# Performance work log

Measured on AMD Instinct MI355X. Metric: run time of the kernel, lower is better.

The kernel has to match this reference:

```python
import jax, jax.numpy as jnp
import numpy as np

KSIZE = 3
KN = (KSIZE - 1) // 2  # 1
TEMP = 50.0


def _extract_patches(x, same_pad):
    """TF tf.image.extract_patches ordering: per location, (dy, dx, channel).
    x: [b,H,W,d] -> [b,h,w,9*d] (h=H,w=W if same_pad else H-2,W-2)."""
    if same_pad:
        x = jnp.pad(x, ((0, 0), (KN, KN), (KN, KN), (0, 0)))
    b, Hp, Wp, d = x.shape
    h, w = Hp - 2 * KN, Wp - 2 * KN
    slices = [x[:, dy:dy + h, dx:dx + w, :]
              for dy in range(KSIZE) for dx in range(KSIZE)]
    return jnp.concatenate(slices, axis=-1)


def setup_inputs() -> dict:
    key = jax.random.key(0)
    k1, k2, k3 = jax.random.split(key, 3)
    b, h, w, dims = 4, 48, 48, 64
    g_in = jax.random.normal(k1, (b, h, w, dims), dtype=jnp.float32)
    # binary inpainting mask (1 = known background, 0 = hole)
    mask = (jax.random.uniform(k2, (b, h, w, 1)) > 0.5).astype(jnp.float32)
    W2 = jax.random.normal(k3, (2 * dims, dims), dtype=jnp.float32) / np.sqrt(2.0 * dims)
    b2 = jnp.zeros((dims,), dtype=jnp.float32)
    return {"g_in": g_in, "mask": mask, "W2": W2, "b2": b2}


def reference(g_in, mask, W2, b2):
    b, h, w, dims = g_in.shape
    c = (h - 2 * KN) * (w - 2 * KN)

    mask_r = mask  # already (h,w,1); broadcasts over dims (== tile)
    bg = g_in * mask_r

    # p1: VALID 3x3 patches of bg -> dynamic kernels, [b, c, 9*dims]
    p1 = _extract_patches(bg, same_pad=False).reshape(b, c, KSIZE * KSIZE * dims)
    # p2: SAME 3x3 patches of g_in, [b, h, w, 9*dims]
    p2 = _extract_patches(g_in, same_pad=True)

    # cross-correlation: conv2d(ft, k1) == per-location dot with each bg patch
    CS = jnp.einsum('byxk,bjk->byxj', p2, p1)              # [b,h,w,c]
    k1d = jnp.sum(p1 * p1, axis=2)                          # [b,c]
    wwd = jnp.sum(p2 * p2, axis=3, keepdims=True)           # [b,h,w,1]
    DS1 = k1d[:, None, None, :] + wwd - 2.0 * CS            # squared distances
    mu = jnp.mean(DS1, axis=3, keepdims=True)
    sd = jnp.std(DS1, axis=3, keepdims=True)                # population std (tf.math.reduce_std)
    DS2 = -jnp.tanh((DS1 - mu) / sd)
    CA = jax.nn.softmax(TEMP * DS2, axis=-1)                # [b,h,w,c]

    # transposed conv aggregation with per-sample kernels k2[b,j,dy,dx,ch]
    k2 = p1.reshape(b, c, KSIZE, KSIZE, dims)
    CA_pad = jnp.pad(CA, ((0, 0), (KN, KN), (KN, KN), (0, 0)))
    acl = jnp.zeros((b, h, w, dims), dtype=g_in.dtype)
    for dy in range(KSIZE):
        for dx in range(KSIZE):
            win = CA_pad[:, 2 * KN - dy:2 * KN - dy + h, 2 * KN - dx:2 * KN - dx + w, :]
            acl = acl + jnp.einsum('byxj,bjd->byxd', win, k2[:, :, dy, dx, :])
    acl = acl / 9.0

    ACL = bg + acl * (1.0 - mask_r)
    con1 = jnp.concatenate([g_in, ACL], axis=3)             # [b,h,w,2*dims]
    return jax.nn.elu(jnp.einsum('byxk,kd->byxd', con1, W2) + b2)
```

## Files before the change

### kernel.cpp

```cpp
#include <hip/hip_runtime.h>
#include <hip/hip_fp16.h>
#include <math.h>

#define BB 4
#define HH 48
#define WW 48
#define DD 64
#define CC 2116
#define HWp (HH*WW)
#define PW 50
#define PP (PW*PW)

#define SLOTW 48
#define NSLOT 2208
#define NGRP 276
#define QW 2304
#define QROWS 2500

typedef __attribute__((ext_vector_type(8))) short short8;
typedef __attribute__((ext_vector_type(8))) _Float16 half8;
typedef __attribute__((ext_vector_type(4))) float float4v;

#define OFFB_GPAD  ((size_t)0)
#define OFFB_BGPAD ((size_t)1280000)
#define OFFB_E     ((size_t)2560000)
#define OFFB_K1D   ((size_t)2596864)
#define OFFB_BGT3  ((size_t)2632192)
#define OFFB_F     ((size_t)6023680)
#define OFFB_CA    ((size_t)52103680)
#define OFFB_CAY   ((size_t)92801536)
#define OFFB_ACLP  ((size_t)133499392)

__device__ __forceinline__ ushort f2bf(float x) {
    unsigned u = __float_as_uint(x);
    return (ushort)((u + 0x7FFFu + ((u >> 16) & 1u)) >> 16);
}

__device__ __forceinline__ float waveReduceSum(float x) {
#pragma unroll
    for (int o = 32; o > 0; o >>= 1) x += __shfl_down(x, o, 64);
    return x;
}

__device__ __forceinline__ __half2 u2h2(uint u) {
    union { uint u; __half2 h; } c; c.u = u; return c.h;
}
__device__ __forceinline__ uint h2u(__half2 h) {
    union { __half2 h; uint u; } c; c.h = h; return c.u;
}

__device__ __forceinline__ uint cvtpk_bf16(float lo, float hi) {
    uint r;
    asm("v_cvt_pk_bf16_f32 %0, %1, %2" : "=v"(r) : "v"(lo), "v"(hi));
    return r;
}

__device__ __forceinline__ float softexp(float d, float mu, float isd) {
    float z = (d - mu) * isd;
    float E2 = __expf(z + z);
    float r = __builtin_amdgcn_rcpf(E2 + 1.f);
    return __expf(fmaf(100.f, r, -50.f));
}

typedef __attribute__((address_space(3))) void lds_void_t;
typedef __attribute__((address_space(1))) void gmem_void_t;
__device__ __forceinline__ void gld16(const ushort* g, ushort* lds) {
    __builtin_amdgcn_global_load_lds((gmem_void_t*)g, (lds_void_t*)lds, 16, 0, 0);
}

__global__ __launch_bounds__(256) void build_pads(const float* __restrict__ g,
                                                  const float* __restrict__ mask,
                                                  ushort* __restrict__ gpad,
                                                  ushort* __restrict__ bgpad,
                                                  float* __restrict__ e) {
    int w = threadIdx.x >> 6, c = threadIdx.x & 63;
    int q4 = blockIdx.x * 4 + w;
    int b = q4 / PP, q = q4 % PP;
    int yp = q / PW, xp = q % PW;
    size_t o = (size_t)q4 * DD + c;
    if (yp >= 1 && yp <= HH && xp >= 1 && xp <= WW) {
        int pix = (yp - 1) * WW + (xp - 1);
        float gv = g[((size_t)b * HWp + pix) * DD + c];
        float m  = mask[(size_t)b * HWp + pix];
        float bgv = gv * m;
        gpad[o]  = f2bf(gv);
        bgpad[o] = f2bf(bgv);
        float ss = waveReduceSum(bgv * bgv);
        if (c == 0) e[b * HWp + pix] = ss;
    } else {
        gpad[o] = 0;
        bgpad[o] = 0;
    }
}

__global__ __launch_bounds__(256) void build_bgt3_k1d(const ushort* __restrict__ bgpad,
                                                      const float* __restrict__ e,
                                                      ushort* __restrict__ bgT3,
                                                      float* __restrict__ k1d) {
    int b = blockIdx.y;
    int t = threadIdx.x;
    if (blockIdx.x == 35) {
#pragma unroll 1
        for (int st = t; st < NSLOT; st += 256) {
            int jy = st / SLOTW, jx = st - jy * SLOTW;
            float s = 0.f;
            if (jx < 46) {
                const float* eb = e + (size_t)b * HWp + jy * WW + jx;
#pragma unroll
                for (int ddy = 0; ddy < 3; ddy++)
#pragma unroll
                    for (int ddx = 0; ddx < 3; ddx++) s += eb[ddy * WW + ddx];
            }
            k1d[(size_t)b * NSLOT + st] = s;
        }
        return;
    }
    __shared__ ushort T[66 * 65];
    int jt = blockIdx.x;
    const ushort* src = bgpad + (size_t)b * PP * DD;
    int lr = t >> 3, c8 = (t & 7) * 8;
#pragma unroll
    for (int pass = 0; pass < 2; pass++) {
        int r = lr + pass * 32;
        int v = jt * 64 + r;
        int vy = v / 48, vx = v - vy * 48;
        uint4 d = *(const uint4*)(src + (size_t)((vy + 1) * PW + (vx + 1)) * DD + c8);
        ushort tmp[8];
        *(uint4*)tmp = d;
#pragma unroll
        for (int u = 0; u < 8; u++) {
            float f = __uint_as_float((uint)tmp[u] << 16);
            __half h = __float2half_rn(f);
            T[r * 65 + c8 + u] = *(ushort*)&h;
        }
    }
    if (t < 16) {
        int r = 64 + (t >> 3);
        int c8b = (t & 7) * 8;
        int v = jt * 64 + r;
        int vy = v / 48, vx = v - vy * 48;
        uint4 d = *(const uint4*)(src + (size_t)((vy + 1) * PW + (vx + 1)) * DD + c8b);
        ushort tmp[8];
        *(uint4*)tmp = d;
#pragma unroll
        for (int u = 0; u < 8; u++) {
            float f = __uint_as_float((uint)tmp[u] << 16);
            __half h = __float2half_rn(f);
            T[r * 65 + c8b + u] = *(ushort*)&h;
        }
    }
    __syncthreads();
#pragma unroll
    for (int pass = 0; pass < 2; pass++) {
        int c = lr + pass * 32;
        int j8 = (t & 7) * 8;
        int col0 = jt * 64 + j8;
        if (col0 < NSLOT) {
#pragma unroll
            for (int dx = 0; dx < 3; dx++) {
                ushort tmp[8];
#pragma unroll
                for (int u = 0; u < 8; u++) tmp[u] = T[(j8 + u + dx) * 65 + c];
                *(uint4*)(bgT3 + ((size_t)b * 192 + dx * 64 + c) * NSLOT + col0) =
                    *(const uint4*)tmp;
            }
        }
    }
}

__global__ __launch_bounds__(256) void fgemm(const ushort* __restrict__ gpad,
                                             const ushort* __restrict__ bgpad,
                                             __half* __restrict__ Fout) {
    __shared__ ushort As[2 * 4096];
    __shared__ ushort Bs[2 * 4096];
    int i0 = blockIdx.x;
    int b = (i0 & 7) >> 1;
    int tile = ((i0 >> 3) << 1) | (i0 & 1);
    int ty = tile / 18, tx = tile - ty * 18;
    int m0 = ty * 128, n0 = tx * 128;
    const ushort* Ag = gpad + (size_t)b * PP * DD;
    const ushort* Bg = bgpad + (size_t)b * PP * DD;

    int tid = threadIdx.x;
    int l = tid & 63, w = tid >> 6;
    int quad = l >> 4, l15 = l & 15;
    int sw8 = (l15 >> 1) & 3;
    int wm = (w >> 1) * 64, wn = (w & 1) * 64;
    int rowInC = l >> 2;
    int cSw = (l & 3) ^ ((l >> 3) & 3);

    int baseA[2], baseB[2];
#pragma unroll
    for (int i = 0; i < 2; i++) {
        int rg = w * 2 + i;
        int r = rg * 16 + rowInC;
        int u = m0 + r; if (u > QROWS - 1) u = QROWS - 1;
        int n = n0 + r;
        int vy = n / 48, vx = n - vy * 48;
        baseA[i] = u * DD + cSw * 8;
        baseB[i] = ((vy + 1) * PW + (vx + 1)) * DD + cSw * 8;
    }

    float4v acc[4][4];
#pragma unroll
    for (int i = 0; i < 4; i++)
#pragma unroll
        for (int j = 0; j < 4; j++) acc[i][j] = (float4v){0.f, 0.f, 0.f, 0.f};

#pragma unroll
    for (int i = 0; i < 2; i++) {
        int rg = w * 2 + i;
        gld16(Ag + baseA[i], As + rg * 512);
        gld16(Bg + baseB[i], Bs + rg * 512);
    }

    int buf = 0;
    for (int k0 = 0; k0 < 192; k0 += 32) {
        __syncthreads();
        int nb = buf ^ 1;
        if (k0 + 32 < 192) {
#pragma unroll
            for (int i = 0; i < 2; i++) {
                int rg = w * 2 + i;
                gld16(Ag + baseA[i] + (k0 + 32), As + nb * 4096 + rg * 512);
                gld16(Bg + baseB[i] + (k0 + 32), Bs + nb * 4096 + rg * 512);
            }
        }
        const ushort* Ax = As + buf * 4096;
        const ushort* Bx = Bs + buf * 4096;
        short8 af[4], bf[4];
#pragma unroll
        for (int i = 0; i < 4; i++)
            af[i] = *(const short8*)&Ax[(wm + i * 16 + l15) * 32 + ((quad ^ sw8)) * 8];
#pragma unroll
        for (int j = 0; j < 4; j++)
            bf[j] = *(const short8*)&Bx[(wn + j * 16 + l15) * 32 + ((quad ^ sw8)) * 8];
#pragma unroll
        for (int i = 0; i < 4; i++)
#pragma unroll
            for (int j = 0; j < 4; j++)
                acc[i][j] = __builtin_amdgcn_mfma_f32_16x16x32_bf16(af[i], bf[j], acc[i][j], 0, 0, 0);
        buf = nb;
    }

    __half* C = Fout + (size_t)b * QROWS * QW;
#pragma unroll
    for (int i = 0; i < 4; i++) {
#pragma unroll
        for (int j = 0; j < 4; j++) {
            int n = n0 + wn + j * 16 + l15;
#pragma unroll
            for (int r = 0; r < 4; r++) {
                int m = m0 + wm + i * 16 + quad * 4 + r;
                if (m < QROWS) C[(size_t)m * QW + n] = __float2half(acc[i][j][r]);
            }
        }
    }
}

__global__ __launch_bounds__(320) void qrowsoft5(const __half* __restrict__ F,
                                                 const float* __restrict__ k1d,
                                                 ushort* __restrict__ CA) {
    __shared__ float red[8][321];
    int i0 = blockIdx.x;
    int b = (i0 & 7) >> 1;
    int sub = ((i0 >> 3) << 1) | (i0 & 1);
    int yq = sub / 48, x = sub - yq * 48;
    int y0 = yq * 4;

    int t = threadIdx.x;
    bool act = (t < NGRP);
    int jy = t / 6, jxb = (t - jy * 6) * 8;
    int slot0 = jy * SLOTW + jxb;
    bool vc6 = act && (jxb == 40);

    __half2 acc[4][4];
#pragma unroll
    for (int p = 0; p < 4; p++)
#pragma unroll
        for (int k = 0; k < 4; k++) acc[p][k] = u2h2(0u);

    float k1v[8] = {0.f, 0.f, 0.f, 0.f, 0.f, 0.f, 0.f, 0.f};

    if (act) {
        const float* k1 = k1d + (size_t)b * NSLOT + slot0;
        float4 ka = *(const float4*)k1;
        float4 kb = *(const float4*)(k1 + 4);
        k1v[0] = ka.x; k1v[1] = ka.y; k1v[2] = ka.z; k1v[3] = ka.w;
        k1v[4] = kb.x; k1v[5] = kb.y; k1v[6] = kb.z; k1v[7] = kb.w;

        const __half* Fb = F + ((size_t)b * QROWS + (size_t)y0 * PW + x) * QW + slot0;
#pragma unroll
        for (int r = 0; r < 6; r++) {
            const __half* R = Fb + (size_t)r * PW * QW;
#pragma unroll
            for (int dy = 0; dy < 3; dy++) {
                int p = r - dy;
                if (p >= 0 && p < 4) {
                    uint4 v4 = *(const uint4*)(R + 48 * dy);
                    acc[p][0] = __hadd2(acc[p][0], u2h2(v4.x));
                    acc[p][1] = __hadd2(acc[p][1], u2h2(v4.y));
                    acc[p][2] = __hadd2(acc[p][2], u2h2(v4.z));
                    acc[p][3] = __hadd2(acc[p][3], u2h2(v4.w));
                }
            }
        }
    }

    if (vc6) {
#pragma unroll
        for (int p = 0; p < 4; p++) acc[p][3] = u2h2(0u);
    }

#pragma unroll
    for (int p = 0; p < 4; p++) {
        float s1p = 0.f, s2p = 0.f;
#pragma unroll
        for (int k = 0; k < 4; k++) {
            float2 f = __half22float2(acc[p][k]);
            float d0 = k1v[2*k]   - 2.f * f.x;
            float d1 = k1v[2*k+1] - 2.f * f.y;
            s1p += d0 + d1;
            s2p = fmaf(d0, d0, fmaf(d1, d1, s2p));
        }
        red[p][t] = s1p;
        red[4 + p][t] = s2p;
    }
    __syncthreads();
    if (t < 128) {
        int v = t >> 4, sb = t & 15;
        float s = 0.f;
#pragma unroll
        for (int k = 0; k < 20; k++) s += red[v][sb + 16 * k];
#pragma unroll
        for (int o = 8; o > 0; o >>= 1) s += __shfl_down(s, o, 16);
        if (sb == 0) red[v][320] = s;
    }
    __syncthreads();
    float mu[4], isd[4];
#pragma unroll
    for (int p = 0; p < 4; p++) {
        float m = red[p][320] * (1.f / (float)CC);
        float ex2 = red[4 + p][320] * (1.f / (float)CC);
        mu[p] = m;
        isd[p] = rsqrtf(ex2 - m * m);
    }

    uint eb[4][4];
#pragma unroll
    for (int p = 0; p < 4; p++) {
        float es = 0.f;
#pragma unroll
        for (int k = 0; k < 4; k++) {
            float2 f = __half22float2(acc[p][k]);
            float d0 = k1v[2*k]   - 2.f * f.x;
            float d1 = k1v[2*k+1] - 2.f * f.y;
            if (k == 3 && vc6) { d0 = 1e9f; d1 = 1e9f; }
            float e0 = softexp(d0, mu[p], isd[p]);
            float e1 = softexp(d1, mu[p], isd[p]);
            es += e0 + e1;
            eb[p][k] = cvtpk_bf16(e0, e1);
        }
        red[p][t] = act ? es : 0.f;
    }
    __syncthreads();
    if (t < 64) {
        int v = t >> 4, sb = t & 15;
        float s = 0.f;
#pragma unroll
        for (int k = 0; k < 20; k++) s += red[v][sb + 16 * k];
#pragma unroll
        for (int o = 8; o > 0; o >>= 1) s += __shfl_down(s, o, 16);
        if (sb == 0) red[v][320] = s;
    }
    __syncthreads();

    if (act) {
#pragma unroll
        for (int p = 0; p < 4; p++) {
            float iz = __builtin_amdgcn_rcpf(red[p][320]);
            uint o[4];
#pragma unroll
            for (int k = 0; k < 4; k++) {
                uint wv = eb[p][k];
                float lo = __uint_as_float(wv << 16) * iz;
                float hi = __uint_as_float(wv & 0xffff0000u) * iz;
                __half2 hh = __halves2half2(__float2half_rn(lo), __float2half_rn(hi));
                o[k] = *(uint*)&hh;
            }
            int pix = (y0 + p) * WW + x;
            ushort* wp = CA + ((size_t)b * HWp + pix) * (size_t)NSLOT + slot0;
            *(uint4*)wp = *(const uint4*)o;
        }
    }
}

__global__ __launch_bounds__(320) void cay_k(const ushort* __restrict__ CAu,
                                             ushort* __restrict__ CAy) {
    int i0 = blockIdx.x;
    int b = (i0 & 7) >> 1;
    int sub = ((i0 >> 3) << 1) | (i0 & 1);
    int y = sub / 12, xt = sub - y * 12;
    int x0 = xt * 4;

    int t = threadIdx.x;
    if (t >= NGRP) return;
    int jy = t / 6, jxb = (t - jy * 6) * 8;
    int slot0 = jy * SLOTW + jxb;

    __half2 acc[4][4];
#pragma unroll
    for (int p = 0; p < 4; p++)
#pragma unroll
        for (int k = 0; k < 4; k++) acc[p][k] = u2h2(0u);

#pragma unroll
    for (int dy = 0; dy < 3; dy++) {
        int yy = y + 1 - dy;
        if (yy < 0 || yy >= 48) continue;
        if (jy < dy) continue;
        const ushort* rp = CAu + ((size_t)b * HWp + yy * 48 + x0) * (size_t)NSLOT
                         + slot0 - 48 * dy;
#pragma unroll
        for (int p = 0; p < 4; p++) {
            uint4 v4 = *(const uint4*)(rp + (size_t)p * NSLOT);
            acc[p][0] = __hadd2(acc[p][0], u2h2(v4.x));
            acc[p][1] = __hadd2(acc[p][1], u2h2(v4.y));
            acc[p][2] = __hadd2(acc[p][2], u2h2(v4.z));
            acc[p][3] = __hadd2(acc[p][3], u2h2(v4.w));
        }
    }

#pragma unroll
    for (int p = 0; p < 4; p++) {
        uint o[4];
#pragma unroll
        for (int k = 0; k < 4; k++) {
            __half2 h = acc[p][k];
            o[k] = *(uint*)&h;
        }
        *(uint4*)(CAy + ((size_t)b * HWp + y * 48 + x0 + p) * (size_t)NSLOT + slot0) =
            *(const uint4*)o;
    }
}

__global__ __launch_bounds__(256) void gemm4s(const ushort* __restrict__ Am,
                                              const ushort* __restrict__ Bm,
                                              __half* __restrict__ aclp) {
    __shared__ ushort As[2 * 4096];
    __shared__ ushort Bs[2 * 6144];
    int i0 = blockIdx.x;
    int b = (i0 & 7) >> 1;
    int t2 = ((i0 >> 3) << 1) | (i0 & 1);
    int s = t2 & 7, mt = t2 >> 3;
    int m0 = mt * 128;
    const int KB[9] = {0, 288, 576, 864, 1152, 1440, 1696, 1952, 2208};
    int kb = KB[s], ke = KB[s + 1];
    const ushort* Ab = Am + ((size_t)b * HWp + m0) * (size_t)NSLOT;
    const ushort* Bb = Bm + (size_t)b * 192 * (size_t)NSLOT;

    int tid = threadIdx.x;
    int l = tid & 63, w = tid >> 6;
    int quad = l >> 4, l15 = l & 15;
    int sw8 = (l15 >> 1) & 3;
    int wm = (w >> 1) * 64, wn = (w & 1) * 96;
    int rowInC = l >> 2;
    int cSw = (l & 3) ^ ((l >> 3) & 3);
    int cS8 = cSw * 8;

    float4v acc[4][6];
#pragma unroll
    for (int i = 0; i < 4; i++)
#pragma unroll
        for (int j = 0; j < 6; j++) acc[i][j] = (float4v){0.f, 0.f, 0.f, 0.f};

#pragma unroll
    for (int i = 0; i < 2; i++) {
        int rg = w * 2 + i;
        gld16(Ab + (size_t)(rg * 16 + rowInC) * NSLOT + kb + cS8, As + rg * 512);
    }
#pragma unroll
    for (int i = 0; i < 3; i++) {
        int rg = w * 3 + i;
        gld16(Bb + (size_t)(rg * 16 + rowInC) * NSLOT + kb + cS8, Bs + rg * 512);
    }

    int buf = 0;
    for (int k0 = kb; k0 < ke; k0 += 32) {
        __syncthreads();
        int nb = buf ^ 1;
        if (k0 + 32 < ke) {
#pragma unroll
            for (int i = 0; i < 2; i++) {
                int rg = w * 2 + i;
                gld16(Ab + (size_t)(rg * 16 + rowInC) * NSLOT + (k0 + 32) + cS8,
                      As + nb * 4096 + rg * 512);
            }
#pragma unroll
            for (int i = 0; i < 3; i++) {
                int rg = w * 3 + i;
                gld16(Bb + (size_t)(rg * 16 + rowInC) * NSLOT + (k0 + 32) + cS8,
                      Bs + nb * 6144 + rg * 512);
            }
        }
        const ushort* Ax = As + buf * 4096;
        const ushort* Bx = Bs + buf * 6144;
        half8 af[4], bf[6];
#pragma unroll
        for (int i = 0; i < 4; i++)
            af[i] = *(const half8*)&Ax[(wm + i * 16 + l15) * 32 + ((quad ^ sw8)) * 8];
#pragma unroll
        for (int j = 0; j < 6; j++)
            bf[j] = *(const half8*)&Bx[(wn + j * 16 + l15) * 32 + ((quad ^ sw8)) * 8];
#pragma unroll
        for (int i = 0; i < 4; i++)
#pragma unroll
            for (int j = 0; j < 6; j++)
                acc[i][j] = __builtin_amdgcn_mfma_f32_16x16x32_f16(af[i], bf[j], acc[i][j], 0, 0, 0);
        buf = nb;
    }

    __half* C = aclp + (size_t)b * HWp * 1536 + (size_t)s * 192;
#pragma unroll
    for (int i = 0; i < 4; i++)
#pragma unroll
        for (int j = 0; j < 6; j++)
#pragma unroll
            for (int r = 0; r < 4; r++) {
                int m = m0 + wm + i * 16 + quad * 4 + r;
                int n = wn + j * 16 + l15;
                C[(size_t)m * 1536 + n] = __float2half(acc[i][j][r]);
            }
}

__global__ __launch_bounds__(256) void final_k5(const float* __restrict__ g,
                                                const float* __restrict__ mask,
                                                const __half* __restrict__ aclp,
                                                const float* __restrict__ W2,
                                                const float* __restrict__ b2,
                                                float* __restrict__ out) {
    int w = threadIdx.x >> 6, d = threadIdx.x & 63;
    int pix = blockIdx.x * 4 + w;
    int b = pix / HWp, yx = pix % HWp;
    int y = yx / WW, x = yx % WW;

    __shared__ float con1[4][128];
    float m = mask[pix];
    float gv = g[(size_t)pix * DD + d];
    float bgv = gv * m;

    float acl = 0.f;
    if (m < 0.5f) {
#pragma unroll
        for (int dx = 0; dx < 3; dx++) {
            int xs = x + 1 - dx;
            if (xs >= 0 && xs < WW) {
                const __half* p = aclp + ((size_t)b * HWp + y * WW + xs) * 1536 + dx * 64 + d;
#pragma unroll
                for (int s = 0; s < 8; s++) acl += __half2float(p[s * 192]);
            }
        }
    }

    float ACL = bgv + (acl / 9.f) * (1.f - m);
    con1[w][d] = gv;
    con1[w][64 + d] = ACL;
    __syncthreads();
    float accv = b2[d];
#pragma unroll 8
    for (int k = 0; k < 128; k++) accv = fmaf(con1[w][k], W2[k * 64 + d], accv);
    out[(size_t)pix * DD + d] = accv > 0.f ? accv : expm1f(accv);
}

extern "C" void kernel_launch(void* const* d_in, const int* in_sizes, int n_in,
                              void* d_out, int out_size, void* d_ws, size_t ws_size,
                              hipStream_t stream) {
    const float* g    = (const float*)d_in[0];
    const float* mask = (const float*)d_in[1];
    const float* W2   = (const float*)d_in[2];
    const float* b2   = (const float*)d_in[3];
    float* out = (float*)d_out;
    char* ws = (char*)d_ws;

    ushort* gpad  = (ushort*)(ws + OFFB_GPAD);
    ushort* bgpad = (ushort*)(ws + OFFB_BGPAD);
    float*  e     = (float*) (ws + OFFB_E);
    float*  k1d   = (float*) (ws + OFFB_K1D);
    ushort* bgT3  = (ushort*)(ws + OFFB_BGT3);
    __half* Fbuf  = (__half*)(ws + OFFB_F);
    ushort* CA    = (ushort*)(ws + OFFB_CA);
    ushort* CAy   = (ushort*)(ws + OFFB_CAY);
    __half* aclp  = (__half*)(ws + OFFB_ACLP);

    build_pads<<<BB * PP / 4, 256, 0, stream>>>(g, mask, gpad, bgpad, e);
    build_bgt3_k1d<<<dim3(36, BB), 256, 0, stream>>>(bgpad, e, bgT3, k1d);

    fgemm<<<1440, 256, 0, stream>>>(gpad, bgpad, Fbuf);
    qrowsoft5<<<BB * HWp / 4, 320, 0, stream>>>(Fbuf, k1d, CA);

    cay_k<<<BB * HWp / 4, 320, 0, stream>>>(CA, CAy);
    gemm4s<<<576, 256, 0, stream>>>(CAy, bgT3, aclp);

    final_k5<<<BB * HWp / 4, 256, 0, stream>>>(g, mask, aclp, W2, b2, out);
}
```

Baseline: 169.7 us.

## Fuse softmax kernel with vertical CA shift-sum via LDS halo recomputation

The row-softmax kernel and the vertical-window accumulation kernel are merged. Each block now computes softmax for 6 rows (4 output rows plus a one-row halo on each side), stores the normalized CA rows in shared memory, and sums them vertically before writing CAy directly. This removes the full CA intermediate buffer round-trip through global memory and one kernel launch. In exchange it recomputes halo rows (1.5x the F reads and softmax work) and adds clamps against a zero variance and a zero normalizer for the out-of-range rows.

```diff
diff --git a/kernel.cpp b/kernel.cpp
--- a/kernel.cpp
+++ b/kernel.cpp
@@ -27,9 +27,8 @@
 #define OFFB_K1D   ((size_t)2596864)
 #define OFFB_BGT3  ((size_t)2632192)
 #define OFFB_F     ((size_t)6023680)
-#define OFFB_CA    ((size_t)52103680)
-#define OFFB_CAY   ((size_t)92801536)
-#define OFFB_ACLP  ((size_t)133499392)
+#define OFFB_CAY   ((size_t)52103680)
+#define OFFB_ACLP  ((size_t)92801536)
 
 __device__ __forceinline__ ushort f2bf(float x) {
     unsigned u = __float_as_uint(x);
@@ -258,10 +257,13 @@
     }
 }
 
-__global__ __launch_bounds__(320) void qrowsoft5(const __half* __restrict__ F,
-                                                 const float* __restrict__ k1d,
-                                                 ushort* __restrict__ CA) {
-    __shared__ float red[8][321];
+__global__ __launch_bounds__(320) void qrscay(const __half* __restrict__ F,
+                                              const float* __restrict__ k1d,
+                                              ushort* __restrict__ CAy) {
+    __shared__ uint smem[6656];
+    float* red = (float*)smem;
+    ushort* calds = (ushort*)smem;
+
     int i0 = blockIdx.x;
     int b = (i0 & 7) >> 1;
     int sub = ((i0 >> 3) << 1) | (i0 & 1);
@@ -274,13 +276,19 @@
     int slot0 = jy * SLOTW + jxb;
     bool vc6 = act && (jxb == 40);
 
-    __half2 acc[4][4];
-#pragma unroll
-    for (int p = 0; p < 4; p++)
-#pragma unroll
-        for (int k = 0; k < 4; k++) acc[p][k] = u2h2(0u);
+    int rowok[6];
+#pragma unroll
+    for (int r = 0; r < 6; r++) {
+        int yr = y0 - 1 + r;
+        rowok[r] = (yr >= 0 && yr < HH) ? 1 : 0;
+    }
 
     float k1v[8] = {0.f, 0.f, 0.f, 0.f, 0.f, 0.f, 0.f, 0.f};
+    __half2 cs[6][4];
+#pragma unroll
+    for (int r = 0; r < 6; r++)
+#pragma unroll
+        for (int k = 0; k < 4; k++) cs[r][k] = u2h2(0u);
 
     if (act) {
         const float* k1 = k1d + (size_t)b * NSLOT + slot0;
@@ -289,158 +297,139 @@
         k1v[0] = ka.x; k1v[1] = ka.y; k1v[2] = ka.z; k1v[3] = ka.w;
         k1v[4] = kb.x; k1v[5] = kb.y; k1v[6] = kb.z; k1v[7] = kb.w;
 
-        const __half* Fb = F + ((size_t)b * QROWS + (size_t)y0 * PW + x) * QW + slot0;
 #pragma unroll
         for (int r = 0; r < 6; r++) {
-            const __half* R = Fb + (size_t)r * PW * QW;
+            if (!rowok[r]) continue;
+            int yr = y0 - 1 + r;
+            const __half* R = F + ((size_t)b * QROWS + (size_t)yr * PW + x) * QW + slot0;
 #pragma unroll
             for (int dy = 0; dy < 3; dy++) {
-                int p = r - dy;
-                if (p >= 0 && p < 4) {
-                    uint4 v4 = *(const uint4*)(R + 48 * dy);
-                    acc[p][0] = __hadd2(acc[p][0], u2h2(v4.x));
-                    acc[p][1] = __hadd2(acc[p][1], u2h2(v4.y));
-                    acc[p][2] = __hadd2(acc[p][2], u2h2(v4.z));
-                    acc[p][3] = __hadd2(acc[p][3], u2h2(v4.w));
-                }
-            }
-        }
-    }
-
+                uint4 v4 = *(const uint4*)(R + (size_t)dy * PW * QW + 48 * dy);
+                cs[r][0] = __hadd2(cs[r][0], u2h2(v4.x));
+                cs[r][1] = __hadd2(cs[r][1], u2h2(v4.y));
+                cs[r][2] = __hadd2(cs[r][2], u2h2(v4.z));
+                cs[r][3] = __hadd2(cs[r][3], u2h2(v4.w));
+            }
+        }
+    }
     if (vc6) {
 #pragma unroll
-        for (int p = 0; p < 4; p++) acc[p][3] = u2h2(0u);
-    }
-
-#pragma unroll
-    for (int p = 0; p < 4; p++) {
+        for (int r = 0; r < 6; r++) cs[r][3] = u2h2(0u);
+    }
+
+#pragma unroll
+    for (int r = 0; r < 6; r++) {
         float s1p = 0.f, s2p = 0.f;
 #pragma unroll
         for (int k = 0; k < 4; k++) {
-            float2 f = __half22float2(acc[p][k]);
+            float2 f = __half22float2(cs[r][k]);
             float d0 = k1v[2*k]   - 2.f * f.x;
             float d1 = k1v[2*k+1] - 2.f * f.y;
             s1p += d0 + d1;
             s2p = fmaf(d0, d0, fmaf(d1, d1, s2p));
         }
-        red[p][t] = s1p;
-        red[4 + p][t] = s2p;
-    }
-    __syncthreads();
-    if (t < 128) {
+        bool live = act && rowok[r];
+        red[r * 321 + t]       = live ? s1p : 0.f;
+        red[(6 + r) * 321 + t] = live ? s2p : 0.f;
+    }
+    __syncthreads();
+    if (t < 192) {
         int v = t >> 4, sb = t & 15;
         float s = 0.f;
 #pragma unroll
-        for (int k = 0; k < 20; k++) s += red[v][sb + 16 * k];
+        for (int k = 0; k < 20; k++) s += red[v * 321 + sb + 16 * k];
 #pragma unroll
         for (int o = 8; o > 0; o >>= 1) s += __shfl_down(s, o, 16);
-        if (sb == 0) red[v][320] = s;
-    }
-    __syncthreads();
-    float mu[4], isd[4];
-#pragma unroll
-    for (int p = 0; p < 4; p++) {
-        float m = red[p][320] * (1.f / (float)CC);
-        float ex2 = red[4 + p][320] * (1.f / (float)CC);
-        mu[p] = m;
-        isd[p] = rsqrtf(ex2 - m * m);
-    }
-
-    uint eb[4][4];
-#pragma unroll
-    for (int p = 0; p < 4; p++) {
+        if (sb == 0) red[v * 321 + 320] = s;
+    }
+    __syncthreads();
+    float mu[6], isd[6];
+#pragma unroll
+    for (int r = 0; r < 6; r++) {
+        float m = red[r * 321 + 320] * (1.f / (float)CC);
+        float ex2 = red[(6 + r) * 321 + 320] * (1.f / (float)CC);
+        mu[r] = m;
+        float var = ex2 - m * m;
+        isd[r] = rsqrtf(var > 1e-20f ? var : 1e-20f);
+    }
+
+    uint eb[6][4];
+#pragma unroll
+    for (int r = 0; r < 6; r++) {
         float es = 0.f;
 #pragma unroll
         for (int k = 0; k < 4; k++) {
-            float2 f = __half22float2(acc[p][k]);
+            float2 f = __half22float2(cs[r][k]);
             float d0 = k1v[2*k]   - 2.f * f.x;
             float d1 = k1v[2*k+1] - 2.f * f.y;
             if (k == 3 && vc6) { d0 = 1e9f; d1 = 1e9f; }
-            float e0 = softexp(d0, mu[p], isd[p]);
-            float e1 = softexp(d1, mu[p], isd[p]);
+            float e0 = softexp(d0, mu[r], isd[r]);
+            float e1 = softexp(d1, mu[r], isd[r]);
             es += e0 + e1;
-            eb[p][k] = cvtpk_bf16(e0, e1);
-        }
-        red[p][t] = act ? es : 0.f;
-    }
-    __syncthreads();
-    if (t < 64) {
+            eb[r][k] = cvtpk_bf16(e0, e1);
+        }
+        red[r * 321 + t] = (act && rowok[r]) ? es : 0.f;
+    }
+    __syncthreads();
+    if (t < 96) {
         int v = t >> 4, sb = t & 15;
         float s = 0.f;
 #pragma unroll
-        for (int k = 0; k < 20; k++) s += red[v][sb + 16 * k];
+        for (int k = 0; k < 20; k++) s += red[v * 321 + sb + 16 * k];
 #pragma unroll
         for (int o = 8; o > 0; o >>= 1) s += __shfl_down(s, o, 16);
-        if (sb == 0) red[v][320] = s;
+        if (sb == 0) red[v * 321 + 320] = s;
+    }
+    __syncthreads();
+    float invz[6];
+#pragma unroll
+    for (int r = 0; r < 6; r++) {
+        float z = red[r * 321 + 320];
+        invz[r] = __builtin_amdgcn_rcpf(z > 0.f ? z : 1.f);
     }
     __syncthreads();
 
     if (act) {
 #pragma unroll
+        for (int r = 0; r < 6; r++) {
+            uint o[4] = {0u, 0u, 0u, 0u};
+            if (rowok[r]) {
+#pragma unroll
+                for (int k = 0; k < 4; k++) {
+                    uint wv = eb[r][k];
+                    float lo = __uint_as_float(wv << 16) * invz[r];
+                    float hi = __uint_as_float(wv & 0xffff0000u) * invz[r];
+                    __half2 hh = __halves2half2(__float2half_rn(lo), __float2half_rn(hi));
+                    o[k] = *(uint*)&hh;
+                }
+            }
+            *(uint4*)&calds[(size_t)r * NSLOT + slot0] = *(const uint4*)o;
+        }
+    }
+    __syncthreads();
+
+    if (act) {
+#pragma unroll
         for (int p = 0; p < 4; p++) {
-            float iz = __builtin_amdgcn_rcpf(red[p][320]);
+            __half2 a[4];
+#pragma unroll
+            for (int k = 0; k < 4; k++) a[k] = u2h2(0u);
+#pragma unroll
+            for (int dy = 0; dy < 3; dy++) {
+                if (jy < dy) continue;
+                int r = p + 2 - dy;
+                uint4 v4 = *(const uint4*)&calds[(size_t)r * NSLOT + slot0 - 48 * dy];
+                a[0] = __hadd2(a[0], u2h2(v4.x));
+                a[1] = __hadd2(a[1], u2h2(v4.y));
+                a[2] = __hadd2(a[2], u2h2(v4.z));
+                a[3] = __hadd2(a[3], u2h2(v4.w));
+            }
             uint o[4];
 #pragma unroll
-            for (int k = 0; k < 4; k++) {
-                uint wv = eb[p][k];
-                float lo = __uint_as_float(wv << 16) * iz;
-                float hi = __uint_as_float(wv & 0xffff0000u) * iz;
-                __half2 hh = __halves2half2(__float2half_rn(lo), __float2half_rn(hi));
-                o[k] = *(uint*)&hh;
-            }
-            int pix = (y0 + p) * WW + x;
-            ushort* wp = CA + ((size_t)b * HWp + pix) * (size_t)NSLOT + slot0;
-            *(uint4*)wp = *(const uint4*)o;
-        }
-    }
-}
-
-__global__ __launch_bounds__(320) void cay_k(const ushort* __restrict__ CAu,
-                                             ushort* __restrict__ CAy) {
-    int i0 = blockIdx.x;
-    int b = (i0 & 7) >> 1;
-    int sub = ((i0 >> 3) << 1) | (i0 & 1);
-    int y = sub / 12, xt = sub - y * 12;
-    int x0 = xt * 4;
-
-    int t = threadIdx.x;
-    if (t >= NGRP) return;
-    int jy = t / 6, jxb = (t - jy * 6) * 8;
-    int slot0 = jy * SLOTW + jxb;
-
-    __half2 acc[4][4];
-#pragma unroll
-    for (int p = 0; p < 4; p++)
-#pragma unroll
-        for (int k = 0; k < 4; k++) acc[p][k] = u2h2(0u);
-
-#pragma unroll
-    for (int dy = 0; dy < 3; dy++) {
-        int yy = y + 1 - dy;
-        if (yy < 0 || yy >= 48) continue;
-        if (jy < dy) continue;
-        const ushort* rp = CAu + ((size_t)b * HWp + yy * 48 + x0) * (size_t)NSLOT
-                         + slot0 - 48 * dy;
-#pragma unroll
-        for (int p = 0; p < 4; p++) {
-            uint4 v4 = *(const uint4*)(rp + (size_t)p * NSLOT);
-            acc[p][0] = __hadd2(acc[p][0], u2h2(v4.x));
-            acc[p][1] = __hadd2(acc[p][1], u2h2(v4.y));
-            acc[p][2] = __hadd2(acc[p][2], u2h2(v4.z));
-            acc[p][3] = __hadd2(acc[p][3], u2h2(v4.w));
-        }
-    }
-
-#pragma unroll
-    for (int p = 0; p < 4; p++) {
-        uint o[4];
-#pragma unroll
-        for (int k = 0; k < 4; k++) {
-            __half2 h = acc[p][k];
-            o[k] = *(uint*)&h;
-        }
-        *(uint4*)(CAy + ((size_t)b * HWp + y * 48 + x0 + p) * (size_t)NSLOT + slot0) =
-            *(const uint4*)o;
+            for (int k = 0; k < 4; k++) o[k] = h2u(a[k]);
+            *(uint4*)(CAy + ((size_t)b * HWp + (y0 + p) * 48 + x) * (size_t)NSLOT + slot0) =
+                *(const uint4*)o;
+        }
     }
 }
 
@@ -588,7 +577,6 @@
     float*  k1d   = (float*) (ws + OFFB_K1D);
     ushort* bgT3  = (ushort*)(ws + OFFB_BGT3);
     __half* Fbuf  = (__half*)(ws + OFFB_F);
-    ushort* CA    = (ushort*)(ws + OFFB_CA);
     ushort* CAy   = (ushort*)(ws + OFFB_CAY);
     __half* aclp  = (__half*)(ws + OFFB_ACLP);
 
@@ -596,9 +584,9 @@
     build_bgt3_k1d<<<dim3(36, BB), 256, 0, stream>>>(bgpad, e, bgT3, k1d);
 
     fgemm<<<1440, 256, 0, stream>>>(gpad, bgpad, Fbuf);
-    qrowsoft5<<<BB * HWp / 4, 320, 0, stream>>>(Fbuf, k1d, CA);
-
-    cay_k<<<BB * HWp / 4, 320, 0, stream>>>(CA, CAy);
+
+    qrscay<<<BB * HWp / 4, 320, 0, stream>>>(Fbuf, k1d, CAy);
+
     gemm4s<<<576, 256, 0, stream>>>(CAy, bgT3, aclp);
 
     final_k5<<<BB * HWp / 4, 256, 0, stream>>>(g, mask, aclp, W2, b2, out);
```

Result: slower. 174.3 us (+2.7%).

## Stage shifted rows in LDS for box-sum and CA y-aggregation kernels

Applied to the files above, without the earlier changes.

The softmax kernel now loads each F row once with coalesced whole-row reads into shared memory, double-buffered through registers, and reads the three dy-shifted windows from LDS rather than issuing three overlapping global loads per row. The CA vertical aggregation kernel is restructured to process 8 output rows per block along one column. It streams 10 input rows through LDS so each input row is read once instead of up to three times. The cost is extra __syncthreads per row, more accumulator registers (8x4 half2), and fewer blocks in the aggregation kernel.

```diff
diff --git a/kernel.cpp b/kernel.cpp
--- a/kernel.cpp
+++ b/kernel.cpp
@@ -258,10 +258,11 @@
     }
 }
 
-__global__ __launch_bounds__(320) void qrowsoft5(const __half* __restrict__ F,
+__global__ __launch_bounds__(320) void qrowsoft6(const __half* __restrict__ F,
                                                  const float* __restrict__ k1d,
                                                  ushort* __restrict__ CA) {
-    __shared__ float red[8][321];
+    __shared__ ushort rowbuf[2304];
+    __shared__ float red[8 * 321];
     int i0 = blockIdx.x;
     int b = (i0 & 7) >> 1;
     int sub = ((i0 >> 3) << 1) | (i0 & 1);
@@ -274,34 +275,46 @@
     int slot0 = jy * SLOTW + jxb;
     bool vc6 = act && (jxb == 40);
 
-    __half2 acc[4][4];
+    __half2 cs[4][4];
 #pragma unroll
     for (int p = 0; p < 4; p++)
 #pragma unroll
-        for (int k = 0; k < 4; k++) acc[p][k] = u2h2(0u);
+        for (int k = 0; k < 4; k++) cs[p][k] = u2h2(0u);
 
     float k1v[8] = {0.f, 0.f, 0.f, 0.f, 0.f, 0.f, 0.f, 0.f};
-
     if (act) {
         const float* k1 = k1d + (size_t)b * NSLOT + slot0;
         float4 ka = *(const float4*)k1;
         float4 kb = *(const float4*)(k1 + 4);
         k1v[0] = ka.x; k1v[1] = ka.y; k1v[2] = ka.z; k1v[3] = ka.w;
         k1v[4] = kb.x; k1v[5] = kb.y; k1v[6] = kb.z; k1v[7] = kb.w;
-
-        const __half* Fb = F + ((size_t)b * QROWS + (size_t)y0 * PW + x) * QW + slot0;
-#pragma unroll
-        for (int r = 0; r < 6; r++) {
-            const __half* R = Fb + (size_t)r * PW * QW;
+    }
+
+    const __half* Fb = F + ((size_t)b * QROWS + (size_t)y0 * PW + x) * QW;
+    uint4 vA = make_uint4(0, 0, 0, 0), vB = make_uint4(0, 0, 0, 0);
+    if (t < 276) vA = *(const uint4*)(Fb + t * 8);
+    if (t < 12)  vB = *(const uint4*)(Fb + 2208 + t * 8);
+#pragma unroll
+    for (int r = 0; r < 6; r++) {
+        if (r > 0) __syncthreads();
+        if (t < 276) *(uint4*)&rowbuf[t * 8] = vA;
+        if (t < 12)  *(uint4*)&rowbuf[2208 + t * 8] = vB;
+        if (r + 1 < 6) {
+            const __half* Rn = Fb + (size_t)(r + 1) * PW * QW;
+            if (t < 276) vA = *(const uint4*)(Rn + t * 8);
+            if (t < 12)  vB = *(const uint4*)(Rn + 2208 + t * 8);
+        }
+        __syncthreads();
+        if (act) {
 #pragma unroll
             for (int dy = 0; dy < 3; dy++) {
                 int p = r - dy;
                 if (p >= 0 && p < 4) {
-                    uint4 v4 = *(const uint4*)(R + 48 * dy);
-                    acc[p][0] = __hadd2(acc[p][0], u2h2(v4.x));
-                    acc[p][1] = __hadd2(acc[p][1], u2h2(v4.y));
-                    acc[p][2] = __hadd2(acc[p][2], u2h2(v4.z));
-                    acc[p][3] = __hadd2(acc[p][3], u2h2(v4.w));
+                    uint4 v4 = *(const uint4*)&rowbuf[slot0 + 48 * dy];
+                    cs[p][0] = __hadd2(cs[p][0], u2h2(v4.x));
+                    cs[p][1] = __hadd2(cs[p][1], u2h2(v4.y));
+                    cs[p][2] = __hadd2(cs[p][2], u2h2(v4.z));
+                    cs[p][3] = __hadd2(cs[p][3], u2h2(v4.w));
                 }
             }
         }
@@ -309,7 +322,7 @@
 
     if (vc6) {
 #pragma unroll
-        for (int p = 0; p < 4; p++) acc[p][3] = u2h2(0u);
+        for (int p = 0; p < 4; p++) cs[p][3] = u2h2(0u);
     }
 
 #pragma unroll
@@ -317,31 +330,31 @@
         float s1p = 0.f, s2p = 0.f;
 #pragma unroll
         for (int k = 0; k < 4; k++) {
-            float2 f = __half22float2(acc[p][k]);
+            float2 f = __half22float2(cs[p][k]);
             float d0 = k1v[2*k]   - 2.f * f.x;
             float d1 = k1v[2*k+1] - 2.f * f.y;
             s1p += d0 + d1;
             s2p = fmaf(d0, d0, fmaf(d1, d1, s2p));
         }
-        red[p][t] = s1p;
-        red[4 + p][t] = s2p;
+        red[p * 321 + t]       = act ? s1p : 0.f;
+        red[(4 + p) * 321 + t] = act ? s2p : 0.f;
     }
     __syncthreads();
     if (t < 128) {
         int v = t >> 4, sb = t & 15;
         float s = 0.f;
 #pragma unroll
-        for (int k = 0; k < 20; k++) s += red[v][sb + 16 * k];
+        for (int k = 0; k < 20; k++) s += red[v * 321 + sb + 16 * k];
 #pragma unroll
         for (int o = 8; o > 0; o >>= 1) s += __shfl_down(s, o, 16);
-        if (sb == 0) red[v][320] = s;
+        if (sb == 0) red[v * 321 + 320] = s;
     }
     __syncthreads();
     float mu[4], isd[4];
 #pragma unroll
     for (int p = 0; p < 4; p++) {
-        float m = red[p][320] * (1.f / (float)CC);
-        float ex2 = red[4 + p][320] * (1.f / (float)CC);
+        float m = red[p * 321 + 320] * (1.f / (float)CC);
+        float ex2 = red[(4 + p) * 321 + 320] * (1.f / (float)CC);
         mu[p] = m;
         isd[p] = rsqrtf(ex2 - m * m);
     }
@@ -352,7 +365,7 @@
         float es = 0.f;
 #pragma unroll
         for (int k = 0; k < 4; k++) {
-            float2 f = __half22float2(acc[p][k]);
+            float2 f = __half22float2(cs[p][k]);
             float d0 = k1v[2*k]   - 2.f * f.x;
             float d1 = k1v[2*k+1] - 2.f * f.y;
             if (k == 3 && vc6) { d0 = 1e9f; d1 = 1e9f; }
@@ -361,24 +374,24 @@
             es += e0 + e1;
             eb[p][k] = cvtpk_bf16(e0, e1);
         }
-        red[p][t] = act ? es : 0.f;
+        red[p * 321 + t] = act ? es : 0.f;
     }
     __syncthreads();
     if (t < 64) {
         int v = t >> 4, sb = t & 15;
         float s = 0.f;
 #pragma unroll
-        for (int k = 0; k < 20; k++) s += red[v][sb + 16 * k];
+        for (int k = 0; k < 20; k++) s += red[v * 321 + sb + 16 * k];
 #pragma unroll
         for (int o = 8; o > 0; o >>= 1) s += __shfl_down(s, o, 16);
-        if (sb == 0) red[v][320] = s;
+        if (sb == 0) red[v * 321 + 320] = s;
     }
     __syncthreads();
 
     if (act) {
 #pragma unroll
         for (int p = 0; p < 4; p++) {
-            float iz = __builtin_amdgcn_rcpf(red[p][320]);
+            float iz = __builtin_amdgcn_rcpf(red[p * 321 + 320]);
             uint o[4];
 #pragma unroll
             for (int k = 0; k < 4; k++) {
@@ -395,52 +408,70 @@
     }
 }
 
-__global__ __launch_bounds__(320) void cay_k(const ushort* __restrict__ CAu,
-                                             ushort* __restrict__ CAy) {
+__global__ __launch_bounds__(320) void cay_k8(const ushort* __restrict__ CAu,
+                                              ushort* __restrict__ CAy) {
+    __shared__ ushort rowbuf[2208];
     int i0 = blockIdx.x;
     int b = (i0 & 7) >> 1;
     int sub = ((i0 >> 3) << 1) | (i0 & 1);
-    int y = sub / 12, xt = sub - y * 12;
-    int x0 = xt * 4;
+    int yo = sub / 48, x = sub - yo * 48;
+    int y0 = yo * 8;
 
     int t = threadIdx.x;
-    if (t >= NGRP) return;
+    bool act = (t < NGRP);
     int jy = t / 6, jxb = (t - jy * 6) * 8;
     int slot0 = jy * SLOTW + jxb;
 
-    __half2 acc[4][4];
-#pragma unroll
-    for (int p = 0; p < 4; p++)
+    const ushort* CAb = CAu + (size_t)b * HWp * (size_t)NSLOT;
+
+    __half2 acc[8][4];
+#pragma unroll
+    for (int p = 0; p < 8; p++)
 #pragma unroll
         for (int k = 0; k < 4; k++) acc[p][k] = u2h2(0u);
 
-#pragma unroll
-    for (int dy = 0; dy < 3; dy++) {
-        int yy = y + 1 - dy;
-        if (yy < 0 || yy >= 48) continue;
-        if (jy < dy) continue;
-        const ushort* rp = CAu + ((size_t)b * HWp + yy * 48 + x0) * (size_t)NSLOT
-                         + slot0 - 48 * dy;
-#pragma unroll
-        for (int p = 0; p < 4; p++) {
-            uint4 v4 = *(const uint4*)(rp + (size_t)p * NSLOT);
-            acc[p][0] = __hadd2(acc[p][0], u2h2(v4.x));
-            acc[p][1] = __hadd2(acc[p][1], u2h2(v4.y));
-            acc[p][2] = __hadd2(acc[p][2], u2h2(v4.z));
-            acc[p][3] = __hadd2(acc[p][3], u2h2(v4.w));
-        }
-    }
-
-#pragma unroll
-    for (int p = 0; p < 4; p++) {
-        uint o[4];
-#pragma unroll
-        for (int k = 0; k < 4; k++) {
-            __half2 h = acc[p][k];
-            o[k] = *(uint*)&h;
-        }
-        *(uint4*)(CAy + ((size_t)b * HWp + y * 48 + x0 + p) * (size_t)NSLOT + slot0) =
-            *(const uint4*)o;
+    uint4 vA = make_uint4(0, 0, 0, 0);
+    {
+        int yy = y0 + 8;
+        if (yy < HH && t < 276)
+            vA = *(const uint4*)(CAb + (size_t)(yy * 48 + x) * NSLOT + t * 8);
+    }
+#pragma unroll
+    for (int r = 9; r >= 0; r--) {
+        if (r < 9) __syncthreads();
+        if (t < 276) *(uint4*)&rowbuf[t * 8] = vA;
+        if (r > 0) {
+            int yy = y0 - 2 + r;
+            vA = make_uint4(0, 0, 0, 0);
+            if (yy >= 0 && yy < HH && t < 276)
+                vA = *(const uint4*)(CAb + (size_t)(yy * 48 + x) * NSLOT + t * 8);
+        }
+        __syncthreads();
+        int yyr = y0 - 1 + r;
+        if (act && yyr >= 0 && yyr < HH) {
+#pragma unroll
+            for (int dy = 0; dy < 3; dy++) {
+                int p = r - 2 + dy;
+                if (p >= 0 && p < 8 && jy >= dy) {
+                    uint4 v4 = *(const uint4*)&rowbuf[slot0 - 48 * dy];
+                    acc[p][0] = __hadd2(acc[p][0], u2h2(v4.x));
+                    acc[p][1] = __hadd2(acc[p][1], u2h2(v4.y));
+                    acc[p][2] = __hadd2(acc[p][2], u2h2(v4.z));
+                    acc[p][3] = __hadd2(acc[p][3], u2h2(v4.w));
+                }
+            }
+        }
+    }
+
+    if (act) {
+#pragma unroll
+        for (int p = 0; p < 8; p++) {
+            uint o[4];
+#pragma unroll
+            for (int k = 0; k < 4; k++) o[k] = h2u(acc[p][k]);
+            *(uint4*)(CAy + ((size_t)b * HWp + (y0 + p) * 48 + x) * (size_t)NSLOT + slot0) =
+                *(const uint4*)o;
+        }
     }
 }
 
@@ -596,9 +627,11 @@
     build_bgt3_k1d<<<dim3(36, BB), 256, 0, stream>>>(bgpad, e, bgT3, k1d);
 
     fgemm<<<1440, 256, 0, stream>>>(gpad, bgpad, Fbuf);
-    qrowsoft5<<<BB * HWp / 4, 320, 0, stream>>>(Fbuf, k1d, CA);
-
-    cay_k<<<BB * HWp / 4, 320, 0, stream>>>(CA, CAy);
+
+    qrowsoft6<<<BB * HWp / 4, 320, 0, stream>>>(Fbuf, k1d, CA);
+
+    cay_k8<<<BB * HWp / 8, 320, 0, stream>>>(CA, CAy);
+
     gemm4s<<<576, 256, 0, stream>>>(CAy, bgT3, aclp);
 
     final_k5<<<BB * HWp / 4, 256, 0, stream>>>(g, mask, aclp, W2, b2, out);
```

Measured after the change: 173.0 us. Within noise of the previous version (+1.9%).
